# Kernel optimization log

Measured on AMD Instinct MI355X. Metric: run time of the kernel, lower is better.

Reference implementation:

```python
import jax, jax.numpy as jnp
import numpy as np

B, T, C, H = 4, 2048, 1024, 16
D = C // H  # head dim = 64

def setup_inputs() -> dict:
    key = jax.random.key(0)
    k1, k2, k3 = jax.random.split(key, 3)
    x = jax.random.normal(k1, (B, T, C), dtype=jnp.float32)
    # torch Linear weight [out,in]; store transposed for x @ W
    W_attn = jax.random.normal(k2, (C, 3 * C), dtype=jnp.float32) * (1.0 / np.sqrt(C))
    W_proj = jax.random.normal(k3, (C, C), dtype=jnp.float32) * (1.0 / np.sqrt(C))
    return {"x": x, "W_attn": W_attn, "W_proj": W_proj}

def reference(x, W_attn, W_proj):
    qkv = x @ W_attn                          # [B,T,3C]
    q, k, v = jnp.split(qkv, 3, axis=-1)
    # [B,T,C] -> [B,H,T,D]
    def heads(t):
        return t.reshape(B, T, H, D).transpose(0, 2, 1, 3)
    q, k, v = heads(q), heads(k), heads(v)
    att = jnp.einsum('bhqd,bhkd->bhqk', q, k) * (1.0 / np.sqrt(D))  # [B,H,T,T]
    causal = jnp.tril(jnp.ones((T, T), dtype=bool))
    att = jnp.where(causal[None, None, :, :], att, -jnp.inf)
    att = jax.nn.softmax(att, axis=-1)
    y = jnp.einsum('bhqk,bhkd->bhqd', att, v)  # [B,H,T,D]
    y = y.transpose(0, 2, 1, 3).reshape(B, T, C)
    return y @ W_proj
```

## Files before the change

kernel.cpp:

```cpp
#include <hip/hip_runtime.h>
#include <hip/hip_bf16.h>

#define BB 4
#define TT 2048
#define CC 1024
#define HH 16
#define DD 64
#define MM (BB*TT)

typedef unsigned short u16;
typedef __bf16 bf16x8 __attribute__((ext_vector_type(8)));
typedef __bf16 bf16x4v __attribute__((ext_vector_type(4)));
typedef u16 u16x8 __attribute__((ext_vector_type(8)));
typedef u16 u16x4 __attribute__((ext_vector_type(4)));
typedef float f32x4 __attribute__((ext_vector_type(4)));

__device__ __forceinline__ u16 f2bf(float f) {
  union { float f; unsigned u; } v; v.f = f;
  unsigned u = v.u;
  return (u16)((u + 0x7fffu + ((u >> 16) & 1u)) >> 16);
}
__device__ __forceinline__ float bf2f(u16 s) {
  union { unsigned u; float f; } v; v.u = ((unsigned)s) << 16; return v.f;
}
__device__ __forceinline__ bf16x8 ld_bf16x8(const u16* p) {
  return *reinterpret_cast<const bf16x8*>(p);
}
__device__ __forceinline__ f32x4 zero4() {
  f32x4 z; z[0] = 0.f; z[1] = 0.f; z[2] = 0.f; z[3] = 0.f; return z;
}

__device__ __forceinline__ void gld_lds16(const u16* g, u16* l) {
  __builtin_amdgcn_global_load_lds(
      (const __attribute__((address_space(1))) void*)g,
      (__attribute__((address_space(3))) void*)l, 16, 0, 0);
}
__device__ __forceinline__ void wait_vm0() { __builtin_amdgcn_s_waitcnt(0x0F70); }

__device__ __forceinline__ float lane_pull(float x, int srclane) {
  int r = __builtin_amdgcn_ds_bpermute(srclane << 2, __builtin_bit_cast(int, x));
  return __builtin_bit_cast(float, r);
}

__global__ void k_cast_bf16(const float* __restrict__ x, u16* __restrict__ o, int n4) {
  int i = blockIdx.x * blockDim.x + threadIdx.x;
  if (i >= n4) return;
  const float4 v = reinterpret_cast<const float4*>(x)[i];
  u16x4 r; r.x = f2bf(v.x); r.y = f2bf(v.y); r.z = f2bf(v.z); r.w = f2bf(v.w);
  reinterpret_cast<u16x4*>(o)[i] = r;
}

__global__ void k_transpose_bf16(const float* __restrict__ W, u16* __restrict__ Wt,
                                 int K, int N) {
  __shared__ float tile[32][33];
  int nb = blockIdx.x * 32, kb = blockIdx.y * 32;
  int tx = threadIdx.x & 31, ty = threadIdx.x >> 5;
  #pragma unroll
  for (int i = ty; i < 32; i += 8)
    tile[i][tx] = W[(size_t)(kb + i) * N + nb + tx];
  __syncthreads();
  #pragma unroll
  for (int i = ty; i < 32; i += 8)
    Wt[(size_t)(nb + i) * K + kb + tx] = f2bf(tile[tx][i]);
}

template<int EPI>
__global__ __launch_bounds__(256, 3)
void k_gemm_bt(const u16* __restrict__ A, const u16* __restrict__ Bt,
               float* __restrict__ outF, u16* __restrict__ qb, u16* __restrict__ kb,
               u16* __restrict__ vt, int N, int K)
{
  __shared__ u16 As[128 * 64];
  __shared__ u16 Bs[128 * 64];
  const int tid  = threadIdx.x;
  const int lane = tid & 63, w = tid >> 6;
  const int l16  = lane & 15, quad = lane >> 4;
  const int wr = w >> 1, wc = w & 1;
  const int m0 = blockIdx.y * 128, n0 = blockIdx.x * 128;
  const int lr8 = lane >> 3, lc8 = lane & 7;

  f32x4 acc[4][4];
  #pragma unroll
  for (int i = 0; i < 4; ++i)
    #pragma unroll
    for (int j = 0; j < 4; ++j) acc[i][j] = zero4();

  for (int k0 = 0; k0 < K; k0 += 64) {
    __syncthreads();
    #pragma unroll
    for (int p = 0; p < 4; ++p) {
      const int row = w * 32 + p * 8 + lr8;
      const int cs  = lc8 ^ (row & 7);
      gld_lds16(A  + (size_t)(m0 + row) * K + k0 + cs * 8, &As[(w * 32 + p * 8) * 64]);
      gld_lds16(Bt + (size_t)(n0 + row) * K + k0 + cs * 8, &Bs[(w * 32 + p * 8) * 64]);
    }
    wait_vm0();
    __syncthreads();
    #pragma unroll
    for (int s = 0; s < 2; ++s) {
      bf16x8 af[4], bfr[4];
      #pragma unroll
      for (int i = 0; i < 4; ++i) {
        int mrow = wr * 64 + i * 16 + l16;
        af[i]  = ld_bf16x8(&As[mrow * 64 + ((s * 4 + quad) ^ (l16 & 7)) * 8]);
        int nrow = wc * 64 + i * 16 + l16;
        bfr[i] = ld_bf16x8(&Bs[nrow * 64 + ((s * 4 + quad) ^ (l16 & 7)) * 8]);
      }
      #pragma unroll
      for (int i = 0; i < 4; ++i)
        #pragma unroll
        for (int j = 0; j < 4; ++j)
          acc[i][j] = __builtin_amdgcn_mfma_f32_16x16x32_bf16(af[i], bfr[j], acc[i][j], 0, 0, 0);
    }
  }

  #pragma unroll
  for (int i = 0; i < 4; ++i) {
    #pragma unroll
    for (int j = 0; j < 4; ++j) {
      const int n = n0 + wc * 64 + j * 16 + l16;
      const int mb = m0 + wr * 64 + i * 16 + quad * 4;
      if (EPI == 0) {
        #pragma unroll
        for (int r = 0; r < 4; ++r)
          outF[(size_t)(mb + r) * N + n] = acc[i][j][r];
      } else {
        const int b = mb >> 11, tb = mb & 2047;
        if (n < CC) {
          const int h = n >> 6, d = n & 63;
          #pragma unroll
          for (int r = 0; r < 4; ++r)
            qb[(((size_t)(b * HH + h) * TT + tb + r) << 6) + d] = f2bf(acc[i][j][r]);
        } else if (n < 2 * CC) {
          const int n2 = n - CC; const int h = n2 >> 6, d = n2 & 63;
          #pragma unroll
          for (int r = 0; r < 4; ++r)
            kb[(((size_t)(b * HH + h) * TT + tb + r) << 6) + d] = f2bf(acc[i][j][r]);
        } else {
          const int n2 = n - 2 * CC; const int h = n2 >> 6, d = n2 & 63;
          u16x4 cv;
          #pragma unroll
          for (int r = 0; r < 4; ++r) cv[r] = f2bf(acc[i][j][r]);
          *reinterpret_cast<u16x4*>(
              vt + ((size_t)(b * HH + h) * DD + d) * TT + tb) = cv;
        }
      }
    }
  }
}

__global__ __launch_bounds__(256, 6)
void k_attn(const u16* __restrict__ qb, const u16* __restrict__ kb,
            const u16* __restrict__ vt, u16* __restrict__ y)
{
  __shared__ u16 Ks[64 * 64];
  __shared__ u16 Vs[64 * 64];
  __shared__ u16 QP[64 * 64];
  const int tid  = threadIdx.x;
  const int lane = tid & 63, w = tid >> 6;
  const int l16  = lane & 15, quad = lane >> 4;
  const int lr8 = lane >> 3, lc8 = lane & 7;

  const int bx = blockIdx.x;
  const int qt = 31 - (bx >> 6);
  const int bh = bx & 63;
  const int h  = bh & 15, b = bh >> 4;

  const u16* qptr = qb + ((size_t)bh * TT + qt * 64) * DD;
  const u16* kptr = kb + (size_t)bh * TT * DD;
  const u16* vptr = vt + (size_t)bh * DD * TT;

  const float qscale = 0.125f * 1.44269504088896340736f;
  #pragma unroll
  for (int p = 0; p < 2; ++p) {
    const int r = w * 16 + p * 8 + lr8;
    u16x8 v = *reinterpret_cast<const u16x8*>(qptr + (size_t)r * DD + lc8 * 8);
    u16x8 o;
    #pragma unroll
    for (int e = 0; e < 8; ++e) o[e] = f2bf(bf2f(v[e]) * qscale);
    *reinterpret_cast<u16x8*>(&QP[r * 64 + (lc8 ^ lr8) * 8]) = o;
  }
  bf16x8 qf[2];
  #pragma unroll
  for (int s = 0; s < 2; ++s)
    qf[s] = ld_bf16x8(&QP[(w * 16 + l16) * 64 + ((s * 4 + quad) ^ (l16 & 7)) * 8]);

  float mrow = -__builtin_inff(), lrow = 0.f;
  f32x4 O[4];
  #pragma unroll
  for (int j = 0; j < 4; ++j) O[j] = zero4();

  const int ktiles = qt + 1;
  for (int kt = 0; kt < ktiles; ++kt) {
    __syncthreads();
    {
      const u16* kt0 = kptr + (size_t)kt * 64 * DD;
      const u16* vt0 = vptr + kt * 64;
      #pragma unroll
      for (int p = 0; p < 2; ++p) {
        const int row = w * 16 + p * 8 + lr8;
        const int cs  = lc8 ^ lr8;
        gld_lds16(kt0 + (size_t)row * DD + cs * 8, &Ks[(w * 16 + p * 8) * 64]);
        gld_lds16(vt0 + (size_t)row * TT + cs * 8, &Vs[(w * 16 + p * 8) * 64]);
      }
    }
    wait_vm0();
    __syncthreads();

    f32x4 St[4];
    #pragma unroll
    for (int j = 0; j < 4; ++j) St[j] = zero4();
    #pragma unroll
    for (int s = 0; s < 2; ++s) {
      #pragma unroll
      for (int j = 0; j < 4; ++j) {
        bf16x8 kfr = ld_bf16x8(&Ks[(j * 16 + l16) * 64 + ((s * 4 + quad) ^ (l16 & 7)) * 8]);
        St[j] = __builtin_amdgcn_mfma_f32_16x16x32_bf16(kfr, qf[s], St[j], 0, 0, 0);
      }
    }
    if (kt == qt) {
      const int qg = w * 16 + l16;
      #pragma unroll
      for (int j = 0; j < 4; ++j)
        #pragma unroll
        for (int r = 0; r < 4; ++r)
          if (j * 16 + quad * 4 + r > qg) St[j][r] = -__builtin_inff();
    }

    float mloc = St[0][0];
    #pragma unroll
    for (int j = 0; j < 4; ++j)
      #pragma unroll
      for (int r = 0; r < 4; ++r) mloc = fmaxf(mloc, St[j][r]);
    mloc = fmaxf(mloc, __shfl_xor(mloc, 16));
    mloc = fmaxf(mloc, __shfl_xor(mloc, 32));
    const float mnew  = fmaxf(mrow, mloc);
    const float alpha = exp2f(mrow - mnew);
    float rsum = 0.f;
    #pragma unroll
    for (int j = 0; j < 4; ++j)
      #pragma unroll
      for (int r = 0; r < 4; ++r) {
        float p = exp2f(St[j][r] - mnew);
        St[j][r] = p;
        rsum += p;
      }
    rsum += __shfl_xor(rsum, 16);
    rsum += __shfl_xor(rsum, 32);
    lrow = lrow * alpha + rsum;
    mrow = mnew;

    f32x4 av;
    #pragma unroll
    for (int r = 0; r < 4; ++r) av[r] = lane_pull(alpha, quad * 4 + r);
    #pragma unroll
    for (int j = 0; j < 4; ++j) O[j] *= av;

    #pragma unroll
    for (int j = 0; j < 4; ++j) {
      union { bf16x4v b; u16x4 u; } cv;
      cv.b[0] = (__bf16)St[j][0]; cv.b[1] = (__bf16)St[j][1];
      cv.b[2] = (__bf16)St[j][2]; cv.b[3] = (__bf16)St[j][3];
      const int c = j * 2 + (quad >> 1);
      const int off = w * 1024 + l16 * 64 + ((c ^ (l16 & 7)) << 3) + ((quad & 1) << 2);
      *reinterpret_cast<u16x4*>(&QP[off]) = cv.u;
    }
    #pragma unroll
    for (int s = 0; s < 2; ++s) {
      bf16x8 pf = ld_bf16x8(&QP[w * 1024 + l16 * 64 + ((s * 4 + quad) ^ (l16 & 7)) * 8]);
      #pragma unroll
      for (int j = 0; j < 4; ++j) {
        bf16x8 vf = ld_bf16x8(&Vs[(j * 16 + l16) * 64 + ((s * 4 + quad) ^ (l16 & 7)) * 8]);
        O[j] = __builtin_amdgcn_mfma_f32_16x16x32_bf16(pf, vf, O[j], 0, 0, 0);
      }
    }
  }

  const float linv = 1.0f / lrow;
  f32x4 lv;
  #pragma unroll
  for (int r = 0; r < 4; ++r) lv[r] = lane_pull(linv, quad * 4 + r);
  #pragma unroll
  for (int j = 0; j < 4; ++j) {
    O[j] *= lv;
    #pragma unroll
    for (int r = 0; r < 4; ++r) {
      int t  = qt * 64 + w * 16 + quad * 4 + r;
      int ch = h * 64 + j * 16 + l16;
      y[(size_t)(b * TT + t) * CC + ch] = f2bf(O[j][r]);
    }
  }
}

extern "C" void kernel_launch(void* const* d_in, const int* in_sizes, int n_in,
                              void* d_out, int out_size, void* d_ws, size_t ws_size,
                              hipStream_t stream) {
  const float* x  = (const float*)d_in[0];
  const float* Wa = (const float*)d_in[1];
  const float* Wp = (const float*)d_in[2];
  float* out = (float*)d_out;

  u16* ws   = (u16*)d_ws;
  u16* xb   = ws;
  u16* Wab  = xb   + (size_t)MM * CC;
  u16* Wpb  = Wab  + (size_t)3 * CC * CC;
  u16* qbuf = Wpb  + (size_t)CC * CC;
  u16* kbuf = qbuf + (size_t)MM * CC;
  u16* vtb  = kbuf + (size_t)MM * CC;
  u16* yb   = vtb  + (size_t)MM * CC;

  k_cast_bf16<<<(MM * CC / 4) / 256, 256, 0, stream>>>(x, xb, MM * CC / 4);
  k_transpose_bf16<<<dim3(3 * CC / 32, CC / 32), 256, 0, stream>>>(Wa, Wab, CC, 3 * CC);
  k_transpose_bf16<<<dim3(CC / 32, CC / 32), 256, 0, stream>>>(Wp, Wpb, CC, CC);
  k_gemm_bt<1><<<dim3(3 * CC / 128, MM / 128), 256, 0, stream>>>(
      xb, Wab, nullptr, qbuf, kbuf, vtb, 3 * CC, CC);
  k_attn<<<64 * 32, 256, 0, stream>>>(qbuf, kbuf, vtb, yb);
  k_gemm_bt<0><<<dim3(CC / 128, MM / 128), 256, 0, stream>>>(
      yb, Wpb, out, nullptr, nullptr, nullptr, CC, CC);
}
```

Measured before the change: 251.5 us.

## Process 128-query tiles per attention block to reuse K/V tiles

The attention kernel now handles 128 query rows per block, with each wave owning 32 rows split into two 16-row MFMA groups, so every loaded K/V tile feeds twice as many queries. This halves the grid and the total K/V global-to-LDS traffic and barrier count per query. Waves whose rows lie entirely before a K tile skip its compute. In exchange, register pressure rises (launch bounds drop to 4 waves per SIMD), LDS per block grows, and there are fewer blocks with more causal imbalance between them.

```diff
diff --git a/kernel.cpp b/kernel.cpp
--- a/kernel.cpp
+++ b/kernel.cpp
@@ -149,48 +149,57 @@
   }
 }
 
-__global__ __launch_bounds__(256, 6)
+__global__ __launch_bounds__(256, 4)
 void k_attn(const u16* __restrict__ qb, const u16* __restrict__ kb,
             const u16* __restrict__ vt, u16* __restrict__ y)
 {
   __shared__ u16 Ks[64 * 64];
   __shared__ u16 Vs[64 * 64];
-  __shared__ u16 QP[64 * 64];
+  __shared__ u16 QP[128 * 64];
   const int tid  = threadIdx.x;
   const int lane = tid & 63, w = tid >> 6;
   const int l16  = lane & 15, quad = lane >> 4;
   const int lr8 = lane >> 3, lc8 = lane & 7;
 
   const int bx = blockIdx.x;
-  const int qt = 31 - (bx >> 6);
+  const int qt = 15 - (bx >> 6);
   const int bh = bx & 63;
   const int h  = bh & 15, b = bh >> 4;
 
-  const u16* qptr = qb + ((size_t)bh * TT + qt * 64) * DD;
+  const u16* qptr = qb + ((size_t)bh * TT + qt * 128) * DD;
   const u16* kptr = kb + (size_t)bh * TT * DD;
   const u16* vptr = vt + (size_t)bh * DD * TT;
 
   const float qscale = 0.125f * 1.44269504088896340736f;
   #pragma unroll
-  for (int p = 0; p < 2; ++p) {
-    const int r = w * 16 + p * 8 + lr8;
+  for (int p = 0; p < 4; ++p) {
+    const int r = p * 32 + (tid >> 3);
     u16x8 v = *reinterpret_cast<const u16x8*>(qptr + (size_t)r * DD + lc8 * 8);
     u16x8 o;
     #pragma unroll
     for (int e = 0; e < 8; ++e) o[e] = f2bf(bf2f(v[e]) * qscale);
-    *reinterpret_cast<u16x8*>(&QP[r * 64 + (lc8 ^ lr8) * 8]) = o;
-  }
-  bf16x8 qf[2];
-  #pragma unroll
-  for (int s = 0; s < 2; ++s)
-    qf[s] = ld_bf16x8(&QP[(w * 16 + l16) * 64 + ((s * 4 + quad) ^ (l16 & 7)) * 8]);
-
-  float mrow = -__builtin_inff(), lrow = 0.f;
-  f32x4 O[4];
-  #pragma unroll
-  for (int j = 0; j < 4; ++j) O[j] = zero4();
-
-  const int ktiles = qt + 1;
+    *reinterpret_cast<u16x8*>(&QP[r * 64 + (lc8 ^ (r & 7)) * 8]) = o;
+  }
+  __syncthreads();
+  bf16x8 qf[2][2];
+  #pragma unroll
+  for (int m = 0; m < 2; ++m)
+    #pragma unroll
+    for (int s = 0; s < 2; ++s)
+      qf[m][s] = ld_bf16x8(&QP[(w * 32 + m * 16 + l16) * 64 +
+                               ((s * 4 + quad) ^ (l16 & 7)) * 8]);
+
+  const int qlo = qt * 128 + w * 32;
+  float mrow[2], lrow[2];
+  f32x4 O[2][4];
+  #pragma unroll
+  for (int m = 0; m < 2; ++m) {
+    mrow[m] = -__builtin_inff(); lrow[m] = 0.f;
+    #pragma unroll
+    for (int j = 0; j < 4; ++j) O[m][j] = zero4();
+  }
+
+  const int ktiles = 2 * qt + 2;
   for (int kt = 0; kt < ktiles; ++kt) {
     __syncthreads();
     {
@@ -199,7 +208,7 @@
       #pragma unroll
       for (int p = 0; p < 2; ++p) {
         const int row = w * 16 + p * 8 + lr8;
-        const int cs  = lc8 ^ lr8;
+        const int cs  = lc8 ^ (row & 7);
         gld_lds16(kt0 + (size_t)row * DD + cs * 8, &Ks[(w * 16 + p * 8) * 64]);
         gld_lds16(vt0 + (size_t)row * TT + cs * 8, &Vs[(w * 16 + p * 8) * 64]);
       }
@@ -207,87 +216,109 @@
     wait_vm0();
     __syncthreads();
 
-    f32x4 St[4];
-    #pragma unroll
-    for (int j = 0; j < 4; ++j) St[j] = zero4();
-    #pragma unroll
-    for (int s = 0; s < 2; ++s) {
-      #pragma unroll
-      for (int j = 0; j < 4; ++j) {
-        bf16x8 kfr = ld_bf16x8(&Ks[(j * 16 + l16) * 64 + ((s * 4 + quad) ^ (l16 & 7)) * 8]);
-        St[j] = __builtin_amdgcn_mfma_f32_16x16x32_bf16(kfr, qf[s], St[j], 0, 0, 0);
-      }
-    }
-    if (kt == qt) {
-      const int qg = w * 16 + l16;
-      #pragma unroll
-      for (int j = 0; j < 4; ++j)
-        #pragma unroll
-        for (int r = 0; r < 4; ++r)
-          if (j * 16 + quad * 4 + r > qg) St[j][r] = -__builtin_inff();
-    }
-
-    float mloc = St[0][0];
-    #pragma unroll
-    for (int j = 0; j < 4; ++j)
-      #pragma unroll
-      for (int r = 0; r < 4; ++r) mloc = fmaxf(mloc, St[j][r]);
-    mloc = fmaxf(mloc, __shfl_xor(mloc, 16));
-    mloc = fmaxf(mloc, __shfl_xor(mloc, 32));
-    const float mnew  = fmaxf(mrow, mloc);
-    const float alpha = exp2f(mrow - mnew);
-    float rsum = 0.f;
-    #pragma unroll
-    for (int j = 0; j < 4; ++j)
+    if (kt * 64 <= qlo + 31) {
+      f32x4 St[2][4];
+      #pragma unroll
+      for (int m = 0; m < 2; ++m)
+        #pragma unroll
+        for (int j = 0; j < 4; ++j) St[m][j] = zero4();
+      #pragma unroll
+      for (int s = 0; s < 2; ++s) {
+        #pragma unroll
+        for (int j = 0; j < 4; ++j) {
+          bf16x8 kfr = ld_bf16x8(&Ks[(j * 16 + l16) * 64 +
+                                     ((s * 4 + quad) ^ (l16 & 7)) * 8]);
+          St[0][j] = __builtin_amdgcn_mfma_f32_16x16x32_bf16(kfr, qf[0][s], St[0][j], 0, 0, 0);
+          St[1][j] = __builtin_amdgcn_mfma_f32_16x16x32_bf16(kfr, qf[1][s], St[1][j], 0, 0, 0);
+        }
+      }
+      if (kt * 64 + 63 > qlo) {
+        #pragma unroll
+        for (int m = 0; m < 2; ++m) {
+          const int qg = qlo + m * 16 + l16;
+          #pragma unroll
+          for (int j = 0; j < 4; ++j)
+            #pragma unroll
+            for (int r = 0; r < 4; ++r)
+              if (kt * 64 + j * 16 + quad * 4 + r > qg) St[m][j][r] = -__builtin_inff();
+        }
+      }
+
+      #pragma unroll
+      for (int m = 0; m < 2; ++m) {
+        float mloc = St[m][0][0];
+        #pragma unroll
+        for (int j = 0; j < 4; ++j)
+          #pragma unroll
+          for (int r = 0; r < 4; ++r) mloc = fmaxf(mloc, St[m][j][r]);
+        mloc = fmaxf(mloc, __shfl_xor(mloc, 16));
+        mloc = fmaxf(mloc, __shfl_xor(mloc, 32));
+        const float mnew  = fmaxf(mrow[m], mloc);
+        const float alpha = exp2f(mrow[m] - mnew);
+        float rsum = 0.f;
+        #pragma unroll
+        for (int j = 0; j < 4; ++j)
+          #pragma unroll
+          for (int r = 0; r < 4; ++r) {
+            float p = exp2f(St[m][j][r] - mnew);
+            St[m][j][r] = p;
+            rsum += p;
+          }
+        rsum += __shfl_xor(rsum, 16);
+        rsum += __shfl_xor(rsum, 32);
+        lrow[m] = lrow[m] * alpha + rsum;
+        mrow[m] = mnew;
+
+        f32x4 av;
+        #pragma unroll
+        for (int r = 0; r < 4; ++r) av[r] = lane_pull(alpha, quad * 4 + r);
+        #pragma unroll
+        for (int j = 0; j < 4; ++j) O[m][j] *= av;
+
+        const int pbase = (w * 2 + m) * 1024;
+        #pragma unroll
+        for (int j = 0; j < 4; ++j) {
+          union { bf16x4v bv; u16x4 u; } cv;
+          cv.bv[0] = (__bf16)St[m][j][0]; cv.bv[1] = (__bf16)St[m][j][1];
+          cv.bv[2] = (__bf16)St[m][j][2]; cv.bv[3] = (__bf16)St[m][j][3];
+          const int c = j * 2 + (quad >> 1);
+          const int off = pbase + l16 * 64 + ((c ^ (l16 & 7)) << 3) + ((quad & 1) << 2);
+          *reinterpret_cast<u16x4*>(&QP[off]) = cv.u;
+        }
+      }
+
+      #pragma unroll
+      for (int s = 0; s < 2; ++s) {
+        bf16x8 pf0 = ld_bf16x8(&QP[(w * 2 + 0) * 1024 + l16 * 64 +
+                                   ((s * 4 + quad) ^ (l16 & 7)) * 8]);
+        bf16x8 pf1 = ld_bf16x8(&QP[(w * 2 + 1) * 1024 + l16 * 64 +
+                                   ((s * 4 + quad) ^ (l16 & 7)) * 8]);
+        #pragma unroll
+        for (int j = 0; j < 4; ++j) {
+          bf16x8 vf = ld_bf16x8(&Vs[(j * 16 + l16) * 64 +
+                                    ((s * 4 + quad) ^ (l16 & 7)) * 8]);
+          O[0][j] = __builtin_amdgcn_mfma_f32_16x16x32_bf16(pf0, vf, O[0][j], 0, 0, 0);
+          O[1][j] = __builtin_amdgcn_mfma_f32_16x16x32_bf16(pf1, vf, O[1][j], 0, 0, 0);
+        }
+      }
+    }
+  }
+
+  #pragma unroll
+  for (int m = 0; m < 2; ++m) {
+    const float linv = 1.0f / lrow[m];
+    f32x4 lv;
+    #pragma unroll
+    for (int r = 0; r < 4; ++r) lv[r] = lane_pull(linv, quad * 4 + r);
+    #pragma unroll
+    for (int j = 0; j < 4; ++j) {
+      O[m][j] *= lv;
       #pragma unroll
       for (int r = 0; r < 4; ++r) {
-        float p = exp2f(St[j][r] - mnew);
-        St[j][r] = p;
-        rsum += p;
-      }
-    rsum += __shfl_xor(rsum, 16);
-    rsum += __shfl_xor(rsum, 32);
-    lrow = lrow * alpha + rsum;
-    mrow = mnew;
-
-    f32x4 av;
-    #pragma unroll
-    for (int r = 0; r < 4; ++r) av[r] = lane_pull(alpha, quad * 4 + r);
-    #pragma unroll
-    for (int j = 0; j < 4; ++j) O[j] *= av;
-
-    #pragma unroll
-    for (int j = 0; j < 4; ++j) {
-      union { bf16x4v b; u16x4 u; } cv;
-      cv.b[0] = (__bf16)St[j][0]; cv.b[1] = (__bf16)St[j][1];
-      cv.b[2] = (__bf16)St[j][2]; cv.b[3] = (__bf16)St[j][3];
-      const int c = j * 2 + (quad >> 1);
-      const int off = w * 1024 + l16 * 64 + ((c ^ (l16 & 7)) << 3) + ((quad & 1) << 2);
-      *reinterpret_cast<u16x4*>(&QP[off]) = cv.u;
-    }
-    #pragma unroll
-    for (int s = 0; s < 2; ++s) {
-      bf16x8 pf = ld_bf16x8(&QP[w * 1024 + l16 * 64 + ((s * 4 + quad) ^ (l16 & 7)) * 8]);
-      #pragma unroll
-      for (int j = 0; j < 4; ++j) {
-        bf16x8 vf = ld_bf16x8(&Vs[(j * 16 + l16) * 64 + ((s * 4 + quad) ^ (l16 & 7)) * 8]);
-        O[j] = __builtin_amdgcn_mfma_f32_16x16x32_bf16(pf, vf, O[j], 0, 0, 0);
-      }
-    }
-  }
-
-  const float linv = 1.0f / lrow;
-  f32x4 lv;
-  #pragma unroll
-  for (int r = 0; r < 4; ++r) lv[r] = lane_pull(linv, quad * 4 + r);
-  #pragma unroll
-  for (int j = 0; j < 4; ++j) {
-    O[j] *= lv;
-    #pragma unroll
-    for (int r = 0; r < 4; ++r) {
-      int t  = qt * 64 + w * 16 + quad * 4 + r;
-      int ch = h * 64 + j * 16 + l16;
-      y[(size_t)(b * TT + t) * CC + ch] = f2bf(O[j][r]);
+        int t  = qt * 128 + w * 32 + m * 16 + quad * 4 + r;
+        int ch = h * 64 + j * 16 + l16;
+        y[(size_t)(b * TT + t) * CC + ch] = f2bf(O[m][j][r]);
+      }
     }
   }
 }
@@ -314,7 +345,7 @@
   k_transpose_bf16<<<dim3(CC / 32, CC / 32), 256, 0, stream>>>(Wp, Wpb, CC, CC);
   k_gemm_bt<1><<<dim3(3 * CC / 128, MM / 128), 256, 0, stream>>>(
       xb, Wab, nullptr, qbuf, kbuf, vtb, 3 * CC, CC);
-  k_attn<<<64 * 32, 256, 0, stream>>>(qbuf, kbuf, vtb, yb);
+  k_attn<<<64 * 16, 256, 0, stream>>>(qbuf, kbuf, vtb, yb);
   k_gemm_bt<0><<<dim3(CC / 128, MM / 128), 256, 0, stream>>>(
       yb, Wpb, out, nullptr, nullptr, nullptr, CC, CC);
 }
```

Result: slower. 344.2 us (+36.8%).
